# Optimization experiments

Measured on AMD Instinct MI355X. Metric: run time of the kernel, lower is better.

## Reference

```python
import jax, jax.numpy as jnp
import numpy as np

N, E, IN, HID, H = 20000, 320000, 256, 128, 4
NEG_SLOPE = 0.2
BN_EPS = 1e-5


def _glorot(k, shape):
    lim = float(np.sqrt(6.0 / (shape[0] + shape[-1])))
    return jax.random.uniform(k, shape, jnp.float32, -lim, lim)


def setup_inputs() -> dict:
    key = jax.random.key(0)
    ks = jax.random.split(key, 16)
    x = jax.random.normal(ks[0], (N, IN), jnp.float32)
    src = jax.random.randint(ks[1], (E,), 0, N, jnp.int32)
    dst = jax.random.randint(ks[2], (E,), 0, N, jnp.int32)
    dst = jnp.where(dst == src, (dst + 1) % N, dst)  # no pre-existing self-loops
    edge_index = jnp.stack([src, dst])
    p = {}
    i = 3
    for l, fin in [(0, IN), (1, HID)]:
        p[f"Wl{l}"] = _glorot(ks[i], (fin, H * HID)); i += 1
        p[f"Wr{l}"] = _glorot(ks[i], (fin, H * HID)); i += 1
        p[f"bl{l}"] = jnp.zeros((H * HID,), jnp.float32)
        p[f"br{l}"] = jnp.zeros((H * HID,), jnp.float32)
        p[f"att{l}"] = _glorot(ks[i], (H, HID)); i += 1
        p[f"b{l}"] = jnp.zeros((HID,), jnp.float32)
        p[f"g{l}"] = jnp.ones((HID,), jnp.float32)
        p[f"be{l}"] = jnp.zeros((HID,), jnp.float32)
    p["skip_W"] = _glorot(ks[i], (IN, HID))
    p["skip_b"] = jnp.zeros((HID,), jnp.float32)
    return {"x": x, "edge_index": edge_index, **p}


def _gatv2(x, src, dst, Wl, bl, Wr, br, att, b, n):
    # PyG GATv2Conv, heads=H, concat=False (mean over heads), eval mode (no dropout)
    xl = (x @ Wl + bl).reshape(n, H, HID)   # lin_l (source)
    xr = (x @ Wr + br).reshape(n, H, HID)   # lin_r (target)
    m = xl[src] + xr[dst]                   # [Etot,H,C]
    e = jnp.einsum('ehc,hc->eh', jax.nn.leaky_relu(m, NEG_SLOPE), att)
    emax = jax.ops.segment_max(e, dst, num_segments=n)
    a = jnp.exp(e - emax[dst])
    denom = jax.ops.segment_sum(a, dst, num_segments=n)
    alpha = a / denom[dst]                  # per-target softmax over incoming edges
    out = jax.ops.segment_sum(alpha[:, :, None] * xl[src], dst, num_segments=n)
    return out.mean(axis=1) + b


def _bn(x, g, be):
    # BatchNorm1d, training-mode batch statistics (biased variance)
    mu = x.mean(0)
    var = x.var(0)
    return (x - mu) * jax.lax.rsqrt(var + BN_EPS) * g + be


def reference(x, edge_index, Wl0, Wr0, bl0, br0, att0, b0, g0, be0,
              Wl1, Wr1, bl1, br1, att1, b1, g1, be1, skip_W, skip_b):
    n = x.shape[0]
    loop = jnp.arange(n, dtype=edge_index.dtype)  # add_self_loops (GATv2 default)
    src = jnp.concatenate([edge_index[0], loop])
    dst = jnp.concatenate([edge_index[1], loop])
    h = x @ skip_W + skip_b
    out = _gatv2(x, src, dst, Wl0, bl0, Wr0, br0, att0, b0, n)
    out = _bn(jax.nn.leaky_relu(out, NEG_SLOPE), g0, be0) + h
    out = _gatv2(out, src, dst, Wl1, bl1, Wr1, br1, att1, b1, n)
    out = _bn(jax.nn.leaky_relu(out, NEG_SLOPE), g1, be1)
    return out
```

## Files before the change

kernel.cpp:

```cpp
#include <hip/hip_runtime.h>
#include <math.h>

#define NEG 0.2f
#define BN_EPS 1e-5f
#define LOG2E 1.44269504088896340736f

typedef __attribute__((ext_vector_type(8))) short  bf16x8;
typedef __attribute__((ext_vector_type(4))) float  f32x4;

__device__ inline unsigned short f2b(float f) {
    unsigned int u = __float_as_uint(f);
    unsigned int r = (u + 0x7fffu + ((u >> 16) & 1u)) >> 16;
    return (unsigned short)r;
}
__device__ inline float b2f_lo(unsigned int u) { return __uint_as_float(u << 16); }
__device__ inline float b2f_hi(unsigned int u) { return __uint_as_float(u & 0xffff0000u); }

__device__ inline unsigned int cvt_pk_bf16(float lo, float hi) {
    unsigned int r;
    asm("v_cvt_pk_bf16_f32 %0, %1, %2" : "=v"(r) : "v"(lo), "v"(hi));
    return r;
}

template<int CTRL>
__device__ inline float dpp_add(float x) {
    int y = __builtin_amdgcn_update_dpp(0, __float_as_int(x), CTRL, 0xF, 0xF, true);
    return x + __int_as_float(y);
}

__global__ void pscan_kernel(const int* __restrict__ counts, int* __restrict__ offsets,
                             int* __restrict__ btot, int n) {
    __shared__ int wsums[16];
    int tid = threadIdx.x, wid = tid >> 6, lane = tid & 63;
    int i = blockIdx.x * 1024 + tid;
    int v = (i < n) ? counts[i] + 1 : 0;
    int incl = v;
#pragma unroll
    for (int off = 1; off < 64; off <<= 1) {
        int t = __shfl_up(incl, off);
        if (lane >= off) incl += t;
    }
    if (lane == 63) wsums[wid] = incl;
    __syncthreads();
    if (tid < 16) {
        int wv = wsums[tid];
        int winc = wv;
#pragma unroll
        for (int off = 1; off < 16; off <<= 1) {
            int t = __shfl_up(winc, off);
            if (tid >= off) winc += t;
        }
        wsums[tid] = winc - wv;
        if (tid == 15) btot[blockIdx.x] = winc;
    }
    __syncthreads();
    if (i < n) offsets[i] = wsums[wid] + incl - v;
}

__global__ void addb_kernel(int* __restrict__ offsets, const int* __restrict__ btot,
                            int n, int nb) {
    __shared__ int sbase;
    if (threadIdx.x == 0) {
        int b = 0, t = 0;
        for (int j = 0; j < nb; ++j) {
            int v = btot[j];
            if (j < (int)blockIdx.x) b += v;
            t += v;
        }
        sbase = b;
        if (blockIdx.x == (unsigned)(nb - 1)) offsets[n] = t;
    }
    __syncthreads();
    int i = blockIdx.x * 1024 + threadIdx.x;
    if (i < n) offsets[i] += sbase;
}

__global__ void scatter_kernel(const int* __restrict__ src, const int* __restrict__ dst,
                               const int* __restrict__ offsets, int* __restrict__ cursor,
                               int* __restrict__ csr_src, int E, int N) {
    int i = blockIdx.x * 256 + threadIdx.x;
    if (i < E) {
        int d = dst[i];
        int pos = offsets[d] + 1 + atomicAdd(&cursor[d], 1);
        csr_src[pos] = src[i];
    } else if (i < E + N) {
        int n = i - E;
        csr_src[offsets[n]] = n;
    }
}

__device__ inline void pack_body(const float* __restrict__ W, unsigned short* __restrict__ Ap,
                                 int K, int Nsrc, int fn_off, int t) {
    int KS = K >> 5;
    int lane = t & 63;
    int frag = t >> 6;
    int ks = frag % KS;
    int nb = frag / KS;
    int fn = fn_off + nb;
    int k0 = ks * 32 + (lane >> 4) * 8;
    int col = nb * 16 + (lane & 15);
    unsigned short o[8];
#pragma unroll
    for (int j = 0; j < 8; ++j) o[j] = f2b(W[(size_t)(k0 + j) * Nsrc + col]);
    *(uint4*)&Ap[(((size_t)fn * KS + ks) * 64 + lane) * 8] = *(uint4*)o;
}

__global__ void prep_kernel(const float* __restrict__ x, unsigned short* __restrict__ xbf,
                            const int* __restrict__ dst, int* __restrict__ counts, int E4,
                            const float* __restrict__ Wl0, const float* __restrict__ Wr0,
                            const float* __restrict__ skW, const float* __restrict__ Wl1,
                            const float* __restrict__ Wr1,
                            unsigned short* __restrict__ Ap0, unsigned short* __restrict__ Ap1,
                            const float* __restrict__ bl0, const float* __restrict__ br0,
                            const float* __restrict__ skb, const float* __restrict__ bl1,
                            const float* __restrict__ br1,
                            float* __restrict__ bias0f, float* __restrict__ bias1f, int N) {
    const int CONV = (N / 16) * 8 / 4;
    int b = blockIdx.x, tid = threadIdx.x;
    int wid = tid >> 6, lane = tid & 63;
    if (b < CONV) {
        int wt = b * 4 + wid;
        int ntile = wt >> 3, ks = wt & 7;
        int r = ntile * 16 + (lane & 15);
        int k = ks * 32 + (lane >> 4) * 8;
        const float4* p = (const float4*)&x[(size_t)r * 256 + k];
        float4 a = p[0], c = p[1];
        unsigned short o[8];
        o[0] = f2b(a.x); o[1] = f2b(a.y); o[2] = f2b(a.z); o[3] = f2b(a.w);
        o[4] = f2b(c.x); o[5] = f2b(c.y); o[6] = f2b(c.z); o[7] = f2b(c.w);
        *(uint4*)&xbf[(((size_t)ntile * 8 + ks) * 64 + lane) * 8] = *(uint4*)o;
        return;
    }
    b -= CONV;
    if (b < 313) {
        int i = b * 256 + tid;
        if (i < E4) {
            int4 d = ((const int4*)dst)[i];
            atomicAdd(&counts[d.x], 1);
            atomicAdd(&counts[d.y], 1);
            atomicAdd(&counts[d.z], 1);
            atomicAdd(&counts[d.w], 1);
        }
        return;
    }
    b -= 313;
    if (b < 64)  { pack_body(Wl0, Ap0, 256, 512, 0,  b * 256 + tid); return; }
    b -= 64;
    if (b < 64)  { pack_body(Wr0, Ap0, 256, 512, 32, b * 256 + tid); return; }
    b -= 64;
    if (b < 16)  { pack_body(skW, Ap0, 256, 128, 64, b * 256 + tid); return; }
    b -= 16;
    if (b < 32)  { pack_body(Wl1, Ap1, 128, 512, 0,  b * 256 + tid); return; }
    b -= 32;
    if (b < 32)  { pack_body(Wr1, Ap1, 128, 512, 32, b * 256 + tid); return; }
    b -= 32;
    {
        int i = b * 256 + tid;
        if (i < 1152) {
            float v = (i < 512) ? bl0[i] : (i < 1024 ? br0[i - 512] : skb[i - 1024]);
            bias0f[i] = v;
        } else if (i < 1152 + 1024) {
            int j = i - 1152;
            bias1f[j] = (j < 512) ? bl1[j] : br1[j - 512];
        }
    }
}

__global__ __launch_bounds__(256) void gemm_nt(
    const unsigned short* __restrict__ Bf, const unsigned short* __restrict__ Ap,
    const float* __restrict__ bias, unsigned short* __restrict__ out,
    int Mnodes, int Ncols, int K) {
    int wid = threadIdx.x >> 6, lane = threadIdx.x & 63;
    int g = lane >> 4, c15 = lane & 15;
    int cfbase = blockIdx.y * 8 + (wid & 1) * 4;
    int ch0 = cfbase * 16;
    int nodeBase = blockIdx.x * 256 + (wid >> 1) * 128;
    const int KS = K >> 5;
    const int lastNT = (Mnodes - 1) >> 4;

    f32x4 acc[4][8];
#pragma unroll
    for (int i = 0; i < 4; ++i)
#pragma unroll
        for (int j = 0; j < 8; ++j) acc[i][j] = (f32x4){0.f, 0.f, 0.f, 0.f};

    int nt[8], nd[8];
#pragma unroll
    for (int nf = 0; nf < 8; ++nf) {
        int t = (nodeBase >> 4) + nf;
        nt[nf] = t < lastNT ? t : lastNT;
        nd[nf] = nodeBase + nf * 16 + c15;
    }

    for (int ks = 0; ks < KS; ++ks) {
        bf16x8 a[4];
#pragma unroll
        for (int mf = 0; mf < 4; ++mf)
            a[mf] = *(const bf16x8*)&Ap[(((size_t)(cfbase + mf) * KS + ks) * 64 + lane) * 8];
        bf16x8 b[8];
#pragma unroll
        for (int nf = 0; nf < 8; ++nf)
            b[nf] = *(const bf16x8*)&Bf[(((size_t)nt[nf] * KS + ks) * 64 + lane) * 8];
#pragma unroll
        for (int nf = 0; nf < 8; ++nf)
#pragma unroll
            for (int mf = 0; mf < 4; ++mf)
                acc[mf][nf] = __builtin_amdgcn_mfma_f32_16x16x32_bf16(a[mf], b[nf], acc[mf][nf], 0, 0, 0);
    }
#pragma unroll
    for (int mf = 0; mf < 4; ++mf) {
        int ch = ch0 + mf * 16 + g * 4;
        float4 bs = *(const float4*)&bias[ch];
#pragma unroll
        for (int nf = 0; nf < 8; ++nf) {
            f32x4 v = acc[mf][nf];
            unsigned int p0 = cvt_pk_bf16(v[0] + bs.x, v[1] + bs.y);
            unsigned int p1 = cvt_pk_bf16(v[2] + bs.z, v[3] + bs.w);
            if (nd[nf] < Mnodes)
                *(uint2*)&out[(size_t)nd[nf] * Ncols + ch] = make_uint2(p0, p1);
        }
    }
}

__global__ __launch_bounds__(64) void gat_edge_kernel(
    const int* __restrict__ offsets, const int* __restrict__ csr_src,
    const unsigned short* __restrict__ base, int stride,
    const float* __restrict__ att, const float* __restrict__ bvec,
    float* __restrict__ prebn, int N) {
    int lane = threadIdx.x;
    int n = blockIdx.x;
    if (n >= N) return;
    int start = offsets[n], e1 = offsets[n + 1] - 1;
    float xrv[8], ca[8], cb[8], bv[8];
    {
        uint4 u = *(const uint4*)&base[(size_t)n * stride + 512 + lane * 8];
        xrv[0] = b2f_lo(u.x); xrv[1] = b2f_hi(u.x);
        xrv[2] = b2f_lo(u.y); xrv[3] = b2f_hi(u.y);
        xrv[4] = b2f_lo(u.z); xrv[5] = b2f_hi(u.z);
        xrv[6] = b2f_lo(u.w); xrv[7] = b2f_hi(u.w);
        const float4* q = (const float4*)&att[lane * 8];
        float4 u0 = q[0], u1 = q[1];
        const float sA = 0.6f * LOG2E, sB = 0.4f * LOG2E;
        ca[0] = u0.x * sA; ca[1] = u0.y * sA; ca[2] = u0.z * sA; ca[3] = u0.w * sA;
        ca[4] = u1.x * sA; ca[5] = u1.y * sA; ca[6] = u1.z * sA; ca[7] = u1.w * sA;
        cb[0] = u0.x * sB; cb[1] = u0.y * sB; cb[2] = u0.z * sB; cb[3] = u0.w * sB;
        cb[4] = u1.x * sB; cb[5] = u1.y * sB; cb[6] = u1.z * sB; cb[7] = u1.w * sB;
        if (lane < 16) {
            const float4* bp = (const float4*)&bvec[lane * 8];
            float4 b0 = bp[0], b1 = bp[1];
            bv[0] = b0.x; bv[1] = b0.y; bv[2] = b0.z; bv[3] = b0.w;
            bv[4] = b1.x; bv[5] = b1.y; bv[6] = b1.z; bv[7] = b1.w;
        }
    }
    float m = -INFINITY, d = 0.f;
    float acc[8] = {0, 0, 0, 0, 0, 0, 0, 0};

    const int lofs = lane * 8;
    auto LD = [&](int j) -> uint4 {
        int jj = j < e1 ? j : e1;
        int s = csr_src[jj];
        return *(const uint4*)&base[(size_t)s * stride + lofs];
    };
    auto PROC = [&](const uint4& Q) {
        float v[8];
        v[0] = b2f_lo(Q.x); v[1] = b2f_hi(Q.x);
        v[2] = b2f_lo(Q.y); v[3] = b2f_hi(Q.y);
        v[4] = b2f_lo(Q.z); v[5] = b2f_hi(Q.z);
        v[6] = b2f_lo(Q.w); v[7] = b2f_hi(Q.w);
        float p = 0.f;
#pragma unroll
        for (int j = 0; j < 8; ++j) {
            float t = v[j] + xrv[j];
            p = fmaf(ca[j], t, fmaf(cb[j], fabsf(t), p));
        }
        p = dpp_add<0xB1>(p);
        p = dpp_add<0x4E>(p);
        p = dpp_add<0x141>(p);
        p = dpp_add<0x140>(p);
        if (__any(p > m)) {
            float mn = fmaxf(m, p);
            float sc = exp2f(m - mn);
            float w = exp2f(p - mn);
            d = fmaf(d, sc, w);
#pragma unroll
            for (int j = 0; j < 8; ++j) acc[j] = fmaf(w, v[j], acc[j] * sc);
            m = mn;
        } else {
            float w = exp2f(p - m);
            d += w;
#pragma unroll
            for (int j = 0; j < 8; ++j) acc[j] = fmaf(w, v[j], acc[j]);
        }
    };

    uint4 q0 = LD(start), q1 = LD(start + 1), q2 = LD(start + 2),
          q3 = LD(start + 3), q4 = LD(start + 4), q5 = LD(start + 5);
    int i = start;
    for (;;) {
        PROC(q0); if (++i > e1) break; q0 = LD(i + 5);
        PROC(q1); if (++i > e1) break; q1 = LD(i + 5);
        PROC(q2); if (++i > e1) break; q2 = LD(i + 5);
        PROC(q3); if (++i > e1) break; q3 = LD(i + 5);
        PROC(q4); if (++i > e1) break; q4 = LD(i + 5);
        PROC(q5); if (++i > e1) break; q5 = LD(i + 5);
    }

    float inv = 1.f / d;
    float t[8];
#pragma unroll
    for (int j = 0; j < 8; ++j) {
        float u = acc[j] * inv;
        u += __shfl_xor(u, 16);
        u += __shfl_xor(u, 32);
        t[j] = u;
    }
    if (lane < 16) {
        float o[8];
#pragma unroll
        for (int j = 0; j < 8; ++j) {
            float v2 = 0.25f * t[j] + bv[j];
            o[j] = v2 > 0.f ? v2 : NEG * v2;
        }
        float* dstp = &prebn[(size_t)n * 128 + lane * 8];
        *(float4*)&dstp[0] = make_float4(o[0], o[1], o[2], o[3]);
        *(float4*)&dstp[4] = make_float4(o[4], o[5], o[6], o[7]);
    }
}

__global__ void bn_stats_kernel(const float* __restrict__ v, float* __restrict__ stats, int N) {
    int c = threadIdx.x;
    int r0 = blockIdx.x * 40;
    int r1 = r0 + 40; if (r1 > N) r1 = N;
    float s = 0.f, ss = 0.f;
    for (int r = r0; r < r1; ++r) {
        float x = v[(size_t)r * 128 + c];
        s += x; ss += x * x;
    }
    atomicAdd(&stats[c], s);
    atomicAdd(&stats[128 + c], ss);
}

__global__ void bn_apply_frag_kernel(const float* __restrict__ v, const float* __restrict__ stats,
                                     const float* __restrict__ g, const float* __restrict__ be,
                                     const unsigned short* __restrict__ skip16, int skipStride,
                                     unsigned short* __restrict__ outf, int N) {
    int wid = threadIdx.x >> 6, lane = threadIdx.x & 63;
    int wt = blockIdx.x * 4 + wid;
    int ntile = wt >> 2, ks = wt & 3;
    int r = ntile * 16 + (lane & 15);
    if (r >= N) return;
    int c = ks * 32 + (lane >> 4) * 8;
    float invN = 1.f / (float)N;
    float4 s0 = *(const float4*)&stats[c],       s1 = *(const float4*)&stats[c + 4];
    float4 q0 = *(const float4*)&stats[128 + c], q1 = *(const float4*)&stats[128 + c + 4];
    float4 g0 = *(const float4*)&g[c],  g1 = *(const float4*)&g[c + 4];
    float4 e0 = *(const float4*)&be[c], e1 = *(const float4*)&be[c + 4];
    float mu[8]   = {s0.x, s0.y, s0.z, s0.w, s1.x, s1.y, s1.z, s1.w};
    float ssum[8] = {q0.x, q0.y, q0.z, q0.w, q1.x, q1.y, q1.z, q1.w};
    float gg[8]   = {g0.x, g0.y, g0.z, g0.w, g1.x, g1.y, g1.z, g1.w};
    float ee[8]   = {e0.x, e0.y, e0.z, e0.w, e1.x, e1.y, e1.z, e1.w};
    const float4* vp = (const float4*)&v[(size_t)r * 128 + c];
    float4 v0 = vp[0], v1 = vp[1];
    float xv[8] = {v0.x, v0.y, v0.z, v0.w, v1.x, v1.y, v1.z, v1.w};
    uint4 sk = *(const uint4*)&skip16[(size_t)r * skipStride + c];
    float skf[8] = {b2f_lo(sk.x), b2f_hi(sk.x), b2f_lo(sk.y), b2f_hi(sk.y),
                    b2f_lo(sk.z), b2f_hi(sk.z), b2f_lo(sk.w), b2f_hi(sk.w)};
    unsigned short o[8];
#pragma unroll
    for (int j = 0; j < 8; ++j) {
        float muj = mu[j] * invN;
        float var = ssum[j] * invN - muj * muj;
        float rs = rsqrtf(var + BN_EPS);
        o[j] = f2b((xv[j] - muj) * rs * gg[j] + ee[j] + skf[j]);
    }
    *(uint4*)&outf[(((size_t)ntile * 4 + ks) * 64 + lane) * 8] = *(uint4*)o;
}

__global__ void bn_apply1_kernel(const float* __restrict__ v, const float* __restrict__ stats,
                                 const float* __restrict__ g, const float* __restrict__ be,
                                 float* __restrict__ outf, int N) {
    int t = blockIdx.x * 256 + threadIdx.x;
    if (t >= N * 16) return;
    int node = t >> 4, c = (t & 15) * 8;
    float invN = 1.f / (float)N;
    const float4* vp = (const float4*)&v[(size_t)node * 128 + c];
    float4 v0 = vp[0], v1 = vp[1];
    float xv[8] = {v0.x, v0.y, v0.z, v0.w, v1.x, v1.y, v1.z, v1.w};
    float4 s0 = *(const float4*)&stats[c],       s1 = *(const float4*)&stats[c + 4];
    float4 q0 = *(const float4*)&stats[128 + c], q1 = *(const float4*)&stats[128 + c + 4];
    float4 g0 = *(const float4*)&g[c],  g1 = *(const float4*)&g[c + 4];
    float4 e0 = *(const float4*)&be[c], e1 = *(const float4*)&be[c + 4];
    float mu[8]   = {s0.x, s0.y, s0.z, s0.w, s1.x, s1.y, s1.z, s1.w};
    float ssum[8] = {q0.x, q0.y, q0.z, q0.w, q1.x, q1.y, q1.z, q1.w};
    float gg[8]   = {g0.x, g0.y, g0.z, g0.w, g1.x, g1.y, g1.z, g1.w};
    float ee[8]   = {e0.x, e0.y, e0.z, e0.w, e1.x, e1.y, e1.z, e1.w};
    float o[8];
#pragma unroll
    for (int j = 0; j < 8; ++j) {
        float muj = mu[j] * invN;
        float var = ssum[j] * invN - muj * muj;
        float rs = rsqrtf(var + BN_EPS);
        o[j] = (xv[j] - muj) * rs * gg[j] + ee[j];
    }
    float4* op = (float4*)&outf[(size_t)node * 128 + c];
    op[0] = make_float4(o[0], o[1], o[2], o[3]);
    op[1] = make_float4(o[4], o[5], o[6], o[7]);
}

extern "C" void kernel_launch(void* const* d_in, const int* in_sizes, int n_in,
                              void* d_out, int out_size, void* d_ws, size_t ws_size,
                              hipStream_t stream) {
    const float* x    = (const float*)d_in[0];
    const int*   ei   = (const int*)d_in[1];
    const float* Wl0  = (const float*)d_in[2];
    const float* Wr0  = (const float*)d_in[3];
    const float* bl0  = (const float*)d_in[4];
    const float* br0  = (const float*)d_in[5];
    const float* att0 = (const float*)d_in[6];
    const float* b0   = (const float*)d_in[7];
    const float* g0   = (const float*)d_in[8];
    const float* be0  = (const float*)d_in[9];
    const float* Wl1  = (const float*)d_in[10];
    const float* Wr1  = (const float*)d_in[11];
    const float* bl1  = (const float*)d_in[12];
    const float* br1  = (const float*)d_in[13];
    const float* att1 = (const float*)d_in[14];
    const float* b1   = (const float*)d_in[15];
    const float* g1   = (const float*)d_in[16];
    const float* be1  = (const float*)d_in[17];
    const float* skW  = (const float*)d_in[18];
    const float* skb  = (const float*)d_in[19];

    const int K0 = 256, K1 = 128;
    int N = in_sizes[0] / K0;
    int E = in_sizes[1] / 2;
    int Etot = E + N;
    int NB = (N + 1023) / 1024;

    char* ws = (char*)d_ws;
    size_t off = 0;
    auto alloc = [&](size_t bytes) { size_t r = off; off += (bytes + 255) & ~(size_t)255; return r; };
    size_t z0 = off;
    int*   counts  = (int*)(ws + alloc((size_t)N * 4));
    int*   cursor  = (int*)(ws + alloc((size_t)N * 4));
    float* stats   = (float*)(ws + alloc(512 * 4));
    size_t z1 = off;
    int*   offsets = (int*)(ws + alloc((size_t)(N + 1) * 4));
    int*   csr_src = (int*)(ws + alloc((size_t)Etot * 4));
    int*   btot    = (int*)(ws + alloc((size_t)NB * 4));
    unsigned short* xbf   = (unsigned short*)(ws + alloc((size_t)N * 256 * 2));
    unsigned short* l0f   = (unsigned short*)(ws + alloc((size_t)N * 128 * 2));
    float* prebn   = (float*)(ws + alloc((size_t)N * 128 * 4));
    unsigned short* fused0 = (unsigned short*)(ws + alloc((size_t)N * 1152 * 2));
    unsigned short* fused1 = fused0;
    unsigned short* Ap0 = (unsigned short*)(ws + alloc((size_t)(1152 / 16) * (K0 / 32) * 64 * 8 * 2));
    unsigned short* Ap1 = (unsigned short*)(ws + alloc((size_t)(1024 / 16) * (K1 / 32) * 64 * 8 * 2));
    float* bias0f = (float*)(ws + alloc(1152 * 4));
    float* bias1f = (float*)(ws + alloc(1024 * 4));
    float* outf = (float*)d_out;

    const int* src = ei;
    const int* dst = ei + E;

    hipMemsetAsync(ws + z0, 0, z1 - z0, stream);

    {
        int CONV = (N / 16) * 8 / 4;
        int nblk = CONV + 313 + 64 + 64 + 16 + 32 + 32 + 9;
        prep_kernel<<<nblk, 256, 0, stream>>>(x, xbf, dst, counts, E / 4,
                                              Wl0, Wr0, skW, Wl1, Wr1, Ap0, Ap1,
                                              bl0, br0, skb, bl1, br1, bias0f, bias1f, N);
    }
    pscan_kernel<<<NB, 1024, 0, stream>>>(counts, offsets, btot, N);
    addb_kernel<<<NB, 1024, 0, stream>>>(offsets, btot, N, NB);
    scatter_kernel<<<(Etot + 255) / 256, 256, 0, stream>>>(src, dst, offsets, cursor, csr_src, E, N);

    {
        dim3 g((N + 255) / 256, 1152 / 128);
        gemm_nt<<<g, 256, 0, stream>>>(xbf, Ap0, bias0f, fused0, N, 1152, K0);
    }
    gat_edge_kernel<<<N, 64, 0, stream>>>(offsets, csr_src, fused0, 1152, att0, b0, prebn, N);
    bn_stats_kernel<<<(N + 39) / 40, 128, 0, stream>>>(prebn, stats, N);
    bn_apply_frag_kernel<<<(N / 16), 256, 0, stream>>>(
        prebn, stats, g0, be0, fused0 + 1024, 1152, l0f, N);

    {
        dim3 g((N + 255) / 256, 1024 / 128);
        gemm_nt<<<g, 256, 0, stream>>>(l0f, Ap1, bias1f, fused1, N, 1024, K1);
    }
    gat_edge_kernel<<<N, 64, 0, stream>>>(offsets, csr_src, fused1, 1024, att1, b1, prebn, N);
    bn_stats_kernel<<<(N + 39) / 40, 128, 0, stream>>>(prebn, stats + 256, N);
    bn_apply1_kernel<<<(N * 16 + 255) / 256, 256, 0, stream>>>(
        prebn, stats + 256, g1, be1, outf, N);
}
```

Baseline: 281.3 us.

## Process two destination nodes per wavefront with interleaved gather pipelines

The GAT edge kernel now handles two target nodes per 64-lane block, interleaving their online-softmax loops so loads for one node overlap compute for the other. Prefetch depth per node drops from six to five, the grid is halved, and launch bounds request four waves per SIMD. This aims to hide gather latency through instruction-level parallelism instead of relying only on occupancy. The cost is higher register pressure, divergent loop tails when degrees differ, and an assumption that N is even.

Measured after the change: 323.8 us. 15.1% more time.

```diff
diff --git a/kernel.cpp b/kernel.cpp
--- a/kernel.cpp
+++ b/kernel.cpp
@@ -222,22 +222,17 @@
     }
 }
 
-__global__ __launch_bounds__(64) void gat_edge_kernel(
+__global__ __launch_bounds__(64, 4) void gat_edge_kernel(
     const int* __restrict__ offsets, const int* __restrict__ csr_src,
     const unsigned short* __restrict__ base, int stride,
     const float* __restrict__ att, const float* __restrict__ bvec,
     float* __restrict__ prebn, int N) {
     int lane = threadIdx.x;
-    int n = blockIdx.x;
-    if (n >= N) return;
-    int start = offsets[n], e1 = offsets[n + 1] - 1;
-    float xrv[8], ca[8], cb[8], bv[8];
-    {
-        uint4 u = *(const uint4*)&base[(size_t)n * stride + 512 + lane * 8];
-        xrv[0] = b2f_lo(u.x); xrv[1] = b2f_hi(u.x);
-        xrv[2] = b2f_lo(u.y); xrv[3] = b2f_hi(u.y);
-        xrv[4] = b2f_lo(u.z); xrv[5] = b2f_hi(u.z);
-        xrv[6] = b2f_lo(u.w); xrv[7] = b2f_hi(u.w);
+    int n0 = blockIdx.x * 2, n1 = n0 + 1;
+    int s0 = offsets[n0], e0 = offsets[n0 + 1] - 1;
+    int s1 = offsets[n1], e1 = offsets[n1 + 1] - 1;
+    float ca[8], cb[8], xr0[8], xr1[8];
+    {
         const float4* q = (const float4*)&att[lane * 8];
         float4 u0 = q[0], u1 = q[1];
         const float sA = 0.6f * LOG2E, sB = 0.4f * LOG2E;
@@ -245,23 +240,33 @@
         ca[4] = u1.x * sA; ca[5] = u1.y * sA; ca[6] = u1.z * sA; ca[7] = u1.w * sA;
         cb[0] = u0.x * sB; cb[1] = u0.y * sB; cb[2] = u0.z * sB; cb[3] = u0.w * sB;
         cb[4] = u1.x * sB; cb[5] = u1.y * sB; cb[6] = u1.z * sB; cb[7] = u1.w * sB;
-        if (lane < 16) {
-            const float4* bp = (const float4*)&bvec[lane * 8];
-            float4 b0 = bp[0], b1 = bp[1];
-            bv[0] = b0.x; bv[1] = b0.y; bv[2] = b0.z; bv[3] = b0.w;
-            bv[4] = b1.x; bv[5] = b1.y; bv[6] = b1.z; bv[7] = b1.w;
-        }
-    }
-    float m = -INFINITY, d = 0.f;
-    float acc[8] = {0, 0, 0, 0, 0, 0, 0, 0};
+        uint4 u = *(const uint4*)&base[(size_t)n0 * stride + 512 + lane * 8];
+        xr0[0] = b2f_lo(u.x); xr0[1] = b2f_hi(u.x);
+        xr0[2] = b2f_lo(u.y); xr0[3] = b2f_hi(u.y);
+        xr0[4] = b2f_lo(u.z); xr0[5] = b2f_hi(u.z);
+        xr0[6] = b2f_lo(u.w); xr0[7] = b2f_hi(u.w);
+        uint4 w = *(const uint4*)&base[(size_t)n1 * stride + 512 + lane * 8];
+        xr1[0] = b2f_lo(w.x); xr1[1] = b2f_hi(w.x);
+        xr1[2] = b2f_lo(w.y); xr1[3] = b2f_hi(w.y);
+        xr1[4] = b2f_lo(w.z); xr1[5] = b2f_hi(w.z);
+        xr1[6] = b2f_lo(w.w); xr1[7] = b2f_hi(w.w);
+    }
+    float m0 = -INFINITY, d0 = 0.f, m1 = -INFINITY, d1 = 0.f;
+    float A0[8] = {0, 0, 0, 0, 0, 0, 0, 0};
+    float A1[8] = {0, 0, 0, 0, 0, 0, 0, 0};
 
     const int lofs = lane * 8;
-    auto LD = [&](int j) -> uint4 {
+    auto LD0 = [&](int j) -> uint4 {
+        int jj = j < e0 ? j : e0;
+        int s = csr_src[jj];
+        return *(const uint4*)&base[(size_t)s * stride + lofs];
+    };
+    auto LD1 = [&](int j) -> uint4 {
         int jj = j < e1 ? j : e1;
         int s = csr_src[jj];
         return *(const uint4*)&base[(size_t)s * stride + lofs];
     };
-    auto PROC = [&](const uint4& Q) {
+    auto PR0 = [&](const uint4& Q) {
         float v[8];
         v[0] = b2f_lo(Q.x); v[1] = b2f_hi(Q.x);
         v[2] = b2f_lo(Q.y); v[3] = b2f_hi(Q.y);
@@ -270,60 +275,126 @@
         float p = 0.f;
 #pragma unroll
         for (int j = 0; j < 8; ++j) {
-            float t = v[j] + xrv[j];
+            float t = v[j] + xr0[j];
             p = fmaf(ca[j], t, fmaf(cb[j], fabsf(t), p));
         }
         p = dpp_add<0xB1>(p);
         p = dpp_add<0x4E>(p);
         p = dpp_add<0x141>(p);
         p = dpp_add<0x140>(p);
-        if (__any(p > m)) {
-            float mn = fmaxf(m, p);
-            float sc = exp2f(m - mn);
+        if (__any(p > m0)) {
+            float mn = fmaxf(m0, p);
+            float sc = exp2f(m0 - mn);
             float w = exp2f(p - mn);
-            d = fmaf(d, sc, w);
-#pragma unroll
-            for (int j = 0; j < 8; ++j) acc[j] = fmaf(w, v[j], acc[j] * sc);
-            m = mn;
+            d0 = fmaf(d0, sc, w);
+#pragma unroll
+            for (int j = 0; j < 8; ++j) A0[j] = fmaf(w, v[j], A0[j] * sc);
+            m0 = mn;
         } else {
-            float w = exp2f(p - m);
-            d += w;
-#pragma unroll
-            for (int j = 0; j < 8; ++j) acc[j] = fmaf(w, v[j], acc[j]);
+            float w = exp2f(p - m0);
+            d0 += w;
+#pragma unroll
+            for (int j = 0; j < 8; ++j) A0[j] = fmaf(w, v[j], A0[j]);
         }
     };
-
-    uint4 q0 = LD(start), q1 = LD(start + 1), q2 = LD(start + 2),
-          q3 = LD(start + 3), q4 = LD(start + 4), q5 = LD(start + 5);
-    int i = start;
-    for (;;) {
-        PROC(q0); if (++i > e1) break; q0 = LD(i + 5);
-        PROC(q1); if (++i > e1) break; q1 = LD(i + 5);
-        PROC(q2); if (++i > e1) break; q2 = LD(i + 5);
-        PROC(q3); if (++i > e1) break; q3 = LD(i + 5);
-        PROC(q4); if (++i > e1) break; q4 = LD(i + 5);
-        PROC(q5); if (++i > e1) break; q5 = LD(i + 5);
-    }
-
-    float inv = 1.f / d;
-    float t[8];
-#pragma unroll
-    for (int j = 0; j < 8; ++j) {
-        float u = acc[j] * inv;
-        u += __shfl_xor(u, 16);
-        u += __shfl_xor(u, 32);
-        t[j] = u;
-    }
+    auto PR1 = [&](const uint4& Q) {
+        float v[8];
+        v[0] = b2f_lo(Q.x); v[1] = b2f_hi(Q.x);
+        v[2] = b2f_lo(Q.y); v[3] = b2f_hi(Q.y);
+        v[4] = b2f_lo(Q.z); v[5] = b2f_hi(Q.z);
+        v[6] = b2f_lo(Q.w); v[7] = b2f_hi(Q.w);
+        float p = 0.f;
+#pragma unroll
+        for (int j = 0; j < 8; ++j) {
+            float t = v[j] + xr1[j];
+            p = fmaf(ca[j], t, fmaf(cb[j], fabsf(t), p));
+        }
+        p = dpp_add<0xB1>(p);
+        p = dpp_add<0x4E>(p);
+        p = dpp_add<0x141>(p);
+        p = dpp_add<0x140>(p);
+        if (__any(p > m1)) {
+            float mn = fmaxf(m1, p);
+            float sc = exp2f(m1 - mn);
+            float w = exp2f(p - mn);
+            d1 = fmaf(d1, sc, w);
+#pragma unroll
+            for (int j = 0; j < 8; ++j) A1[j] = fmaf(w, v[j], A1[j] * sc);
+            m1 = mn;
+        } else {
+            float w = exp2f(p - m1);
+            d1 += w;
+#pragma unroll
+            for (int j = 0; j < 8; ++j) A1[j] = fmaf(w, v[j], A1[j]);
+        }
+    };
+
+    uint4 a0 = LD0(s0), a1 = LD0(s0 + 1), a2 = LD0(s0 + 2), a3 = LD0(s0 + 3), a4 = LD0(s0 + 4);
+    uint4 b0 = LD1(s1), b1 = LD1(s1 + 1), b2 = LD1(s1 + 2), b3 = LD1(s1 + 3), b4 = LD1(s1 + 4);
+    int i0 = s0, i1 = s1;
+    while (i0 <= e0 || i1 <= e1) {
+        if (i0 <= e0) { PR0(a0); ++i0; a0 = LD0(i0 + 4); }
+        if (i1 <= e1) { PR1(b0); ++i1; b0 = LD1(i1 + 4); }
+        if (i0 <= e0) { PR0(a1); ++i0; a1 = LD0(i0 + 4); }
+        if (i1 <= e1) { PR1(b1); ++i1; b1 = LD1(i1 + 4); }
+        if (i0 <= e0) { PR0(a2); ++i0; a2 = LD0(i0 + 4); }
+        if (i1 <= e1) { PR1(b2); ++i1; b2 = LD1(i1 + 4); }
+        if (i0 <= e0) { PR0(a3); ++i0; a3 = LD0(i0 + 4); }
+        if (i1 <= e1) { PR1(b3); ++i1; b3 = LD1(i1 + 4); }
+        if (i0 <= e0) { PR0(a4); ++i0; a4 = LD0(i0 + 4); }
+        if (i1 <= e1) { PR1(b4); ++i1; b4 = LD1(i1 + 4); }
+    }
+
+    float bv[8];
     if (lane < 16) {
-        float o[8];
+        const float4* bp = (const float4*)&bvec[lane * 8];
+        float4 v0 = bp[0], v1 = bp[1];
+        bv[0] = v0.x; bv[1] = v0.y; bv[2] = v0.z; bv[3] = v0.w;
+        bv[4] = v1.x; bv[5] = v1.y; bv[6] = v1.z; bv[7] = v1.w;
+    }
+    {
+        float inv = 1.f / d0;
+        float t[8];
 #pragma unroll
         for (int j = 0; j < 8; ++j) {
-            float v2 = 0.25f * t[j] + bv[j];
-            o[j] = v2 > 0.f ? v2 : NEG * v2;
-        }
-        float* dstp = &prebn[(size_t)n * 128 + lane * 8];
-        *(float4*)&dstp[0] = make_float4(o[0], o[1], o[2], o[3]);
-        *(float4*)&dstp[4] = make_float4(o[4], o[5], o[6], o[7]);
+            float u = A0[j] * inv;
+            u += __shfl_xor(u, 16);
+            u += __shfl_xor(u, 32);
+            t[j] = u;
+        }
+        if (lane < 16) {
+            float o[8];
+#pragma unroll
+            for (int j = 0; j < 8; ++j) {
+                float v2 = 0.25f * t[j] + bv[j];
+                o[j] = v2 > 0.f ? v2 : NEG * v2;
+            }
+            float* dstp = &prebn[(size_t)n0 * 128 + lane * 8];
+            *(float4*)&dstp[0] = make_float4(o[0], o[1], o[2], o[3]);
+            *(float4*)&dstp[4] = make_float4(o[4], o[5], o[6], o[7]);
+        }
+    }
+    {
+        float inv = 1.f / d1;
+        float t[8];
+#pragma unroll
+        for (int j = 0; j < 8; ++j) {
+            float u = A1[j] * inv;
+            u += __shfl_xor(u, 16);
+            u += __shfl_xor(u, 32);
+            t[j] = u;
+        }
+        if (lane < 16) {
+            float o[8];
+#pragma unroll
+            for (int j = 0; j < 8; ++j) {
+                float v2 = 0.25f * t[j] + bv[j];
+                o[j] = v2 > 0.f ? v2 : NEG * v2;
+            }
+            float* dstp = &prebn[(size_t)n1 * 128 + lane * 8];
+            *(float4*)&dstp[0] = make_float4(o[0], o[1], o[2], o[3]);
+            *(float4*)&dstp[4] = make_float4(o[4], o[5], o[6], o[7]);
+        }
     }
 }
 
@@ -479,7 +550,7 @@
         dim3 g((N + 255) / 256, 1152 / 128);
         gemm_nt<<<g, 256, 0, stream>>>(xbf, Ap0, bias0f, fused0, N, 1152, K0);
     }
-    gat_edge_kernel<<<N, 64, 0, stream>>>(offsets, csr_src, fused0, 1152, att0, b0, prebn, N);
+    gat_edge_kernel<<<N / 2, 64, 0, stream>>>(offsets, csr_src, fused0, 1152, att0, b0, prebn, N);
     bn_stats_kernel<<<(N + 39) / 40, 128, 0, stream>>>(prebn, stats, N);
     bn_apply_frag_kernel<<<(N / 16), 256, 0, stream>>>(
         prebn, stats, g0, be0, fused0 + 1024, 1152, l0f, N);
@@ -488,7 +559,7 @@
         dim3 g((N + 255) / 256, 1024 / 128);
         gemm_nt<<<g, 256, 0, stream>>>(l0f, Ap1, bias1f, fused1, N, 1024, K1);
     }
-    gat_edge_kernel<<<N, 64, 0, stream>>>(offsets, csr_src, fused1, 1024, att1, b1, prebn, N);
+    gat_edge_kernel<<<N / 2, 64, 0, stream>>>(offsets, csr_src, fused1, 1024, att1, b1, prebn, N);
     bn_stats_kernel<<<(N + 39) / 40, 128, 0, stream>>>(prebn, stats + 256, N);
     bn_apply1_kernel<<<(N * 16 + 255) / 256, 256, 0, stream>>>(
         prebn, stats + 256, g1, be1, outf, N);
```

## Store pre-BatchNorm activations in bf16 and deepen edge gather prefetch to eight

Applied to the files above, without the earlier changes.

The GAT edge kernel now writes its pre-BatchNorm output as packed bf16 instead of fp32, and the BN stats and both BN apply kernels read bf16. This halves the traffic for that intermediate tensor. The edge loop's software prefetch depth also grows from six to eight outstanding row loads, to hide gather latency better. In exchange, BN statistics are computed on rounded values, which loses some precision, and the deeper prefetch uses more registers.

New measurement: 280.8 us. About the same (-0.2%).

```diff
diff --git a/kernel.cpp b/kernel.cpp
--- a/kernel.cpp
+++ b/kernel.cpp
@@ -226,7 +226,7 @@
     const int* __restrict__ offsets, const int* __restrict__ csr_src,
     const unsigned short* __restrict__ base, int stride,
     const float* __restrict__ att, const float* __restrict__ bvec,
-    float* __restrict__ prebn, int N) {
+    unsigned short* __restrict__ prebn, int N) {
     int lane = threadIdx.x;
     int n = blockIdx.x;
     if (n >= N) return;
@@ -293,16 +293,18 @@
         }
     };
 
-    uint4 q0 = LD(start), q1 = LD(start + 1), q2 = LD(start + 2),
-          q3 = LD(start + 3), q4 = LD(start + 4), q5 = LD(start + 5);
+    uint4 q0 = LD(start),     q1 = LD(start + 1), q2 = LD(start + 2), q3 = LD(start + 3),
+          q4 = LD(start + 4), q5 = LD(start + 5), q6 = LD(start + 6), q7 = LD(start + 7);
     int i = start;
     for (;;) {
-        PROC(q0); if (++i > e1) break; q0 = LD(i + 5);
-        PROC(q1); if (++i > e1) break; q1 = LD(i + 5);
-        PROC(q2); if (++i > e1) break; q2 = LD(i + 5);
-        PROC(q3); if (++i > e1) break; q3 = LD(i + 5);
-        PROC(q4); if (++i > e1) break; q4 = LD(i + 5);
-        PROC(q5); if (++i > e1) break; q5 = LD(i + 5);
+        PROC(q0); if (++i > e1) break; q0 = LD(i + 7);
+        PROC(q1); if (++i > e1) break; q1 = LD(i + 7);
+        PROC(q2); if (++i > e1) break; q2 = LD(i + 7);
+        PROC(q3); if (++i > e1) break; q3 = LD(i + 7);
+        PROC(q4); if (++i > e1) break; q4 = LD(i + 7);
+        PROC(q5); if (++i > e1) break; q5 = LD(i + 7);
+        PROC(q6); if (++i > e1) break; q6 = LD(i + 7);
+        PROC(q7); if (++i > e1) break; q7 = LD(i + 7);
     }
 
     float inv = 1.f / d;
@@ -321,26 +323,31 @@
             float v2 = 0.25f * t[j] + bv[j];
             o[j] = v2 > 0.f ? v2 : NEG * v2;
         }
-        float* dstp = &prebn[(size_t)n * 128 + lane * 8];
-        *(float4*)&dstp[0] = make_float4(o[0], o[1], o[2], o[3]);
-        *(float4*)&dstp[4] = make_float4(o[4], o[5], o[6], o[7]);
-    }
-}
-
-__global__ void bn_stats_kernel(const float* __restrict__ v, float* __restrict__ stats, int N) {
+        uint4 pk;
+        pk.x = cvt_pk_bf16(o[0], o[1]);
+        pk.y = cvt_pk_bf16(o[2], o[3]);
+        pk.z = cvt_pk_bf16(o[4], o[5]);
+        pk.w = cvt_pk_bf16(o[6], o[7]);
+        *(uint4*)&prebn[(size_t)n * 128 + lane * 8] = pk;
+    }
+}
+
+__global__ void bn_stats_kernel(const unsigned short* __restrict__ v,
+                                float* __restrict__ stats, int N) {
     int c = threadIdx.x;
     int r0 = blockIdx.x * 40;
     int r1 = r0 + 40; if (r1 > N) r1 = N;
     float s = 0.f, ss = 0.f;
     for (int r = r0; r < r1; ++r) {
-        float x = v[(size_t)r * 128 + c];
+        float x = b2f_lo((unsigned int)v[(size_t)r * 128 + c]);
         s += x; ss += x * x;
     }
     atomicAdd(&stats[c], s);
     atomicAdd(&stats[128 + c], ss);
 }
 
-__global__ void bn_apply_frag_kernel(const float* __restrict__ v, const float* __restrict__ stats,
+__global__ void bn_apply_frag_kernel(const unsigned short* __restrict__ v,
+                                     const float* __restrict__ stats,
                                      const float* __restrict__ g, const float* __restrict__ be,
                                      const unsigned short* __restrict__ skip16, int skipStride,
                                      unsigned short* __restrict__ outf, int N) {
@@ -359,9 +366,9 @@
     float ssum[8] = {q0.x, q0.y, q0.z, q0.w, q1.x, q1.y, q1.z, q1.w};
     float gg[8]   = {g0.x, g0.y, g0.z, g0.w, g1.x, g1.y, g1.z, g1.w};
     float ee[8]   = {e0.x, e0.y, e0.z, e0.w, e1.x, e1.y, e1.z, e1.w};
-    const float4* vp = (const float4*)&v[(size_t)r * 128 + c];
-    float4 v0 = vp[0], v1 = vp[1];
-    float xv[8] = {v0.x, v0.y, v0.z, v0.w, v1.x, v1.y, v1.z, v1.w};
+    uint4 xu = *(const uint4*)&v[(size_t)r * 128 + c];
+    float xv[8] = {b2f_lo(xu.x), b2f_hi(xu.x), b2f_lo(xu.y), b2f_hi(xu.y),
+                   b2f_lo(xu.z), b2f_hi(xu.z), b2f_lo(xu.w), b2f_hi(xu.w)};
     uint4 sk = *(const uint4*)&skip16[(size_t)r * skipStride + c];
     float skf[8] = {b2f_lo(sk.x), b2f_hi(sk.x), b2f_lo(sk.y), b2f_hi(sk.y),
                     b2f_lo(sk.z), b2f_hi(sk.z), b2f_lo(sk.w), b2f_hi(sk.w)};
@@ -376,16 +383,17 @@
     *(uint4*)&outf[(((size_t)ntile * 4 + ks) * 64 + lane) * 8] = *(uint4*)o;
 }
 
-__global__ void bn_apply1_kernel(const float* __restrict__ v, const float* __restrict__ stats,
+__global__ void bn_apply1_kernel(const unsigned short* __restrict__ v,
+                                 const float* __restrict__ stats,
                                  const float* __restrict__ g, const float* __restrict__ be,
                                  float* __restrict__ outf, int N) {
     int t = blockIdx.x * 256 + threadIdx.x;
     if (t >= N * 16) return;
     int node = t >> 4, c = (t & 15) * 8;
     float invN = 1.f / (float)N;
-    const float4* vp = (const float4*)&v[(size_t)node * 128 + c];
-    float4 v0 = vp[0], v1 = vp[1];
-    float xv[8] = {v0.x, v0.y, v0.z, v0.w, v1.x, v1.y, v1.z, v1.w};
+    uint4 xu = *(const uint4*)&v[(size_t)node * 128 + c];
+    float xv[8] = {b2f_lo(xu.x), b2f_hi(xu.x), b2f_lo(xu.y), b2f_hi(xu.y),
+                   b2f_lo(xu.z), b2f_hi(xu.z), b2f_lo(xu.w), b2f_hi(xu.w)};
     float4 s0 = *(const float4*)&stats[c],       s1 = *(const float4*)&stats[c + 4];
     float4 q0 = *(const float4*)&stats[128 + c], q1 = *(const float4*)&stats[128 + c + 4];
     float4 g0 = *(const float4*)&g[c],  g1 = *(const float4*)&g[c + 4];
@@ -450,7 +458,7 @@
     int*   btot    = (int*)(ws + alloc((size_t)NB * 4));
     unsigned short* xbf   = (unsigned short*)(ws + alloc((size_t)N * 256 * 2));
     unsigned short* l0f   = (unsigned short*)(ws + alloc((size_t)N * 128 * 2));
-    float* prebn   = (float*)(ws + alloc((size_t)N * 128 * 4));
+    unsigned short* prebn = (unsigned short*)(ws + alloc((size_t)N * 128 * 2));
     unsigned short* fused0 = (unsigned short*)(ws + alloc((size_t)N * 1152 * 2));
     unsigned short* fused1 = fused0;
     unsigned short* Ap0 = (unsigned short*)(ws + alloc((size_t)(1152 / 16) * (K0 / 32) * 64 * 8 * 2));
```
